# Performance work log

Measured on AMD Instinct MI355X. Metric: run time of the kernel, lower is better.

Reference implementation:

```python
import jax, jax.numpy as jnp
import numpy as np

D_IN, D_HID, D_CLS, N_CLASSES = 1024, 256, 128, 4
CELL_IN = 512
N = 50000


def setup_inputs() -> dict:
    key = jax.random.key(0)
    ks = jax.random.split(key, 20)
    s = 0.02
    inp = {
        "x_path": jax.random.normal(ks[0], (1, N, D_IN), jnp.float32),
        "x_cell": jax.random.normal(ks[1], (1, N, CELL_IN), jnp.float32),
        # wsi_net / cell_net projections
        "wsi_w": jax.random.normal(ks[2], (D_IN, D_HID), jnp.float32) * s,
        "wsi_b": jnp.zeros((D_HID,), jnp.float32),
        "cell_w": jax.random.normal(ks[3], (CELL_IN, D_HID), jnp.float32) * s,
        "cell_b": jnp.zeros((D_HID,), jnp.float32),
        # cross-attention Q/K/V
        "wq_w": jax.random.normal(ks[4], (D_HID, D_HID), jnp.float32) * s,
        "wq_b": jnp.zeros((D_HID,), jnp.float32),
        "wk_w": jax.random.normal(ks[5], (D_HID, D_HID), jnp.float32) * s,
        "wk_b": jnp.zeros((D_HID,), jnp.float32),
        "wv_w": jax.random.normal(ks[6], (D_HID, D_HID), jnp.float32) * s,
        "wv_b": jnp.zeros((D_HID,), jnp.float32),
        # gated attention (L=D=256, n_classes=1)
        "aa_w": jax.random.normal(ks[7], (D_HID, D_HID), jnp.float32) * s,
        "aa_b": jnp.zeros((D_HID,), jnp.float32),
        "ab_w": jax.random.normal(ks[8], (D_HID, D_HID), jnp.float32) * s,
        "ab_b": jnp.zeros((D_HID,), jnp.float32),
        "ac_w": jax.random.normal(ks[9], (D_HID, 1), jnp.float32) * s,
        "ac_b": jnp.zeros((1,), jnp.float32),
        # classifier MLP
        "c1_w": jax.random.normal(ks[10], (D_HID, D_CLS), jnp.float32) * s,
        "c1_b": jnp.zeros((D_CLS,), jnp.float32),
        "c2_w": jax.random.normal(ks[11], (D_CLS, N_CLASSES), jnp.float32) * s,
        "c2_b": jnp.zeros((N_CLASSES,), jnp.float32),
    }
    return inp


def reference(x_path, x_cell, wsi_w, wsi_b, cell_w, cell_b,
              wq_w, wq_b, wk_w, wk_b, wv_w, wv_b,
              aa_w, aa_b, ab_w, ab_b, ac_w, ac_b,
              c1_w, c1_b, c2_w, c2_b):
    xp = x_path[0]            # (N, D_IN)
    xc = x_cell[0]            # (N, CELL_IN)
    # instance-level projections (dropout inactive at eval)
    h_path = jax.nn.relu(xp @ wsi_w + wsi_b)    # (N, d)
    h_cell = jax.nn.relu(xc @ cell_w + cell_b)  # (N, d)
    # cross attention with per-instance seq_len=1 (bmm over N singleton batches)
    q = h_cell @ wq_w + wq_b
    k = h_path @ wk_w + wk_b
    v = h_path @ wv_w + wv_b
    scores = (jnp.einsum('nd,nd->n', q, k) / jnp.sqrt(jnp.float32(q.shape[-1])))[:, None, None]  # (N,1,1)
    attn_w = jax.nn.softmax(scores, axis=-1)     # (N,1,1), trivially ones
    fused = attn_w[:, 0, :] * v                  # (N, d)
    # gated attention MIL pooling
    a = jnp.tanh(fused @ aa_w + aa_b)
    b = jax.nn.sigmoid(fused @ ab_w + ab_b)
    A = (a * b) @ ac_w + ac_b                    # (N, 1)
    A_t = A.T                                    # (1, N)
    pooled = jax.nn.softmax(A_t, axis=1) @ fused # (1, d)
    # classifier MLP
    risk = jax.nn.relu(pooled @ c1_w + c1_b) @ c2_w + c2_b  # (1, n_classes)
    return risk
```

## Files before the change

kernel.cpp:

```cpp
#include <hip/hip_runtime.h>
#include <hip/hip_bf16.h>
#include <math.h>

#define D_IN 1024
#define D_HID 256
#define D_CLS 128
#define N_CLASSES 4
#define N_INST 50000

#define NPAD 50176
#define G1 (NPAD / 64)
#define RG2 128
#define GB (NPAD / RG2)
#define PSTR 258
#define NEG_BIG (-1e30f)

#define ROWS 64
#define NBLK ((N_INST + ROWS - 1) / ROWS)
#define NB2 64
#define CHUNK ((NBLK + NB2 - 1) / NB2)

#define WS_W1T   0u
#define WS_WVT   524288u
#define WS_WAT   655360u
#define WS_WBT   786432u
#define WS_CNT   917504u
#define WS_P1    917760u
#define WS_H     1322304u
#define WS_NEED2 ((size_t)WS_H + 25690112u)
#define WS_P1F   917504u
#define WS_P2F   1724800u

typedef __attribute__((ext_vector_type(8))) short bf16x8;
typedef __attribute__((ext_vector_type(4))) float f32x4;

__device__ __forceinline__ short f2bf(float x) {
    __hip_bfloat16 h = __float2bfloat16(x);
    return *reinterpret_cast<short*>(&h);
}
__device__ __forceinline__ float fast_tanh(float x) {
    float e = __expf(2.f * x);
    return 1.f - 2.f * __builtin_amdgcn_rcpf(e + 1.f);
}
__device__ __forceinline__ float fast_sigmoid(float x) {
    return __builtin_amdgcn_rcpf(1.f + __expf(-x));
}
__device__ __forceinline__ bf16x8 cvt8(float4 a, float4 b) {
    bf16x8 r;
    r[0] = f2bf(a.x); r[1] = f2bf(a.y); r[2] = f2bf(a.z); r[3] = f2bf(a.w);
    r[4] = f2bf(b.x); r[5] = f2bf(b.y); r[6] = f2bf(b.z); r[7] = f2bf(b.w);
    return r;
}
__device__ __forceinline__ bf16x8 cvt8v(f32x4 a, f32x4 b) {
    bf16x8 r;
    r[0] = f2bf(a[0]); r[1] = f2bf(a[1]); r[2] = f2bf(a[2]); r[3] = f2bf(a[3]);
    r[4] = f2bf(b[0]); r[5] = f2bf(b[1]); r[6] = f2bf(b[2]); r[7] = f2bf(b[3]);
    return r;
}
__device__ __forceinline__ bf16x8 load_cvt8(const float* __restrict__ p) {
    return cvt8(*(const float4*)p, *(const float4*)(p + 4));
}
__device__ __forceinline__ void async_ld16(const float* g, float* l) {
    __builtin_amdgcn_global_load_lds(
        (const __attribute__((address_space(1))) void*)g,
        (__attribute__((address_space(3))) void*)l, 16, 0, 0);
}

__global__ void convert_weights(const float* __restrict__ w1, const float* __restrict__ wv,
                                const float* __restrict__ wa, const float* __restrict__ wb,
                                __hip_bfloat16* __restrict__ w1t, __hip_bfloat16* __restrict__ wvt,
                                __hip_bfloat16* __restrict__ wat, __hip_bfloat16* __restrict__ wbt) {
    __shared__ __hip_bfloat16 T[64][68];
    int b = blockIdx.x, tid = threadIdx.x;
    const float* src; __hip_bfloat16* dst; int K, tr, tc;
    if (b < 64) { src = w1; dst = w1t; K = D_IN; tr = b >> 2; tc = b & 3; }
    else {
        int m = (b - 64) >> 4, t = (b - 64) & 15;
        src = (m == 0) ? wv : (m == 1) ? wa : wb;
        dst = (m == 0) ? wvt : (m == 1) ? wat : wbt;
        K = D_HID; tr = t >> 2; tc = t & 3;
    }
    int k0 = tr * 64, n0 = tc * 64;
#pragma unroll
    for (int p = 0; p < 4; p++) {
        int lin = p * 256 + tid;
        int r = lin >> 4;
        int c4 = (lin & 15) << 2;
        float4 v = *(const float4*)(src + (size_t)(k0 + r) * D_HID + n0 + c4);
        T[c4 + 0][r] = __float2bfloat16(v.x);
        T[c4 + 1][r] = __float2bfloat16(v.y);
        T[c4 + 2][r] = __float2bfloat16(v.z);
        T[c4 + 3][r] = __float2bfloat16(v.w);
    }
    __syncthreads();
#pragma unroll
    for (int p = 0; p < 4; p++) {
        int lin = p * 256 + tid;
        int n = lin >> 4;
        int kq = (lin & 15) << 2;
        ushort4 o;
        o.x = *(unsigned short*)&T[n][kq + 0];
        o.y = *(unsigned short*)&T[n][kq + 1];
        o.z = *(unsigned short*)&T[n][kq + 2];
        o.w = *(unsigned short*)&T[n][kq + 3];
        *(ushort4*)(dst + (size_t)(n0 + n) * K + k0 + kq) = o;
    }
}

__global__ __launch_bounds__(256, 3) void mcat_stage1h(const float* __restrict__ xp,
                                                       const __hip_bfloat16* __restrict__ w1t,
                                                       const float* __restrict__ b1,
                                                       __hip_bfloat16* __restrict__ hout) {
    __shared__ float Xs[4][2048];

    const int tid  = threadIdx.x;
    const int wave = tid >> 6;
    const int lane = tid & 63;
    const int quad = lane >> 4;
    const int l16  = lane & 15;
    const int row0 = blockIdx.x * 64;
    const int t128 = blockIdx.x >> 1;
    const int rhalf = blockIdx.x & 1;

    const int dma_rsub = lane >> 3;
    const int dma_gran = (lane & 7) ^ dma_rsub;
    auto stage = [&](int buf, int kc) {
#pragma unroll
        for (int c = 0; c < 2; c++) {
            const int chunk = wave * 2 + c;
            int rg = row0 + chunk * 8 + dma_rsub;
            if (rg > N_INST - 1) rg = N_INST - 1;
            async_ld16(xp + (size_t)rg * D_IN + kc + dma_gran * 4, &Xs[buf][chunk * 256]);
        }
    };

    const __hip_bfloat16* wb[4];
#pragma unroll
    for (int ct = 0; ct < 4; ct++)
        wb[ct] = w1t + (size_t)(wave * 64 + ct * 16 + l16) * D_IN + quad * 8;

    f32x4 acc[4][4];
    f32x4 zero = {0.f, 0.f, 0.f, 0.f};
#pragma unroll
    for (int i = 0; i < 4; i++)
#pragma unroll
        for (int j = 0; j < 4; j++) acc[i][j] = zero;

    stage(0, 0);
    bf16x8 wcur[4];
#pragma unroll
    for (int ct = 0; ct < 4; ct++) wcur[ct] = *(const bf16x8*)(wb[ct]);
    stage(1, 32);
    stage(2, 64);

    const int key = l16 & 7;
#pragma unroll 1
    for (int t = 0; t < 32; t++) {
        if (t == 0)      asm volatile("s_waitcnt vmcnt(4)" ::: "memory");
        else if (t < 29) asm volatile("s_waitcnt vmcnt(2)" ::: "memory");
        else             asm volatile("s_waitcnt vmcnt(0)" ::: "memory");
        __builtin_amdgcn_s_barrier();

        bf16x8 wnx[4];
        if (t < 31) {
#pragma unroll
            for (int ct = 0; ct < 4; ct++)
                wnx[ct] = *(const bf16x8*)(wb[ct] + (t + 1) * 32);
        }
        if (t < 29) stage((t + 3) & 3, (t + 3) * 32);

        const float* bufp = &Xs[t & 3][0];
#pragma unroll
        for (int rt = 0; rt < 4; rt++) {
            const float* rp = bufp + (rt * 16 + l16) * 32;
            f32x4 lo = *(const f32x4*)(rp + (((2 * quad) ^ key) << 2));
            f32x4 hi = *(const f32x4*)(rp + (((2 * quad + 1) ^ key) << 2));
            bf16x8 af = cvt8v(lo, hi);
#pragma unroll
            for (int ct = 0; ct < 4; ct++)
                acc[rt][ct] = __builtin_amdgcn_mfma_f32_16x16x32_bf16(af, wcur[ct], acc[rt][ct], 0, 0, 0);
        }
        if (t < 31) {
#pragma unroll
            for (int ct = 0; ct < 4; ct++) wcur[ct] = wnx[ct];
        }
    }

#pragma unroll
    for (int ct = 0; ct < 4; ct++) {
        const int col = wave * 64 + ct * 16 + l16;
        const float bias = b1[col];
        __hip_bfloat16* hb = hout + (((size_t)(t128 * 8 + (col >> 5)) * 4 + ((col >> 3) & 3)) << 10)
                                  + rhalf * 512 + (col & 7);
#pragma unroll
        for (int rt = 0; rt < 4; rt++)
#pragma unroll
            for (int r = 0; r < 4; r++) {
                int row = rt * 16 + quad * 4 + r;
                hb[row * 8] = __float2bfloat16(fmaxf(acc[rt][ct][r] + bias, 0.f));
            }
    }
}

__global__ __launch_bounds__(512, 1) void mcat_stage2(const __hip_bfloat16* __restrict__ h,
                          const __hip_bfloat16* __restrict__ wvt, const float* __restrict__ bv,
                          const __hip_bfloat16* __restrict__ wat, const float* __restrict__ ba,
                          const __hip_bfloat16* __restrict__ wbt, const float* __restrict__ bb,
                          const float* __restrict__ acw, const float* __restrict__ acb,
                          float* __restrict__ p1, unsigned int* __restrict__ counter,
                          const float* __restrict__ c1w, const float* __restrict__ c1b,
                          const float* __restrict__ c2w, const float* __restrict__ c2b,
                          float* __restrict__ out) {
    __shared__ __hip_bfloat16 Vs[RG2][264];
    __shared__ float Apart[8][RG2];
    __shared__ float ExpW[RG2];
    __shared__ float smx[4];
    __shared__ float scb[GB];
    __shared__ float pooled[D_HID];
    __shared__ float r1v[D_CLS];

    const int tid  = threadIdx.x;
    const int wave = tid >> 6;
    const int lane = tid & 63;
    const int quad = lane >> 4;
    const int l16  = lane & 15;
    const int cb   = wave * 32;
    const int row0 = blockIdx.x * RG2;

    f32x4 acc[8][2];
    f32x4 zero = {0.f, 0.f, 0.f, 0.f};

    const __hip_bfloat16* hb = h + (size_t)blockIdx.x * 32768 + quad * 1024 + l16 * 8;
#pragma unroll
    for (int i = 0; i < 8; i++) { acc[i][0] = zero; acc[i][1] = zero; }
    {
        const __hip_bfloat16* w0 = wvt + (size_t)(cb + l16) * D_HID + quad * 8;
        const __hip_bfloat16* w1p = w0 + 16 * D_HID;
#pragma unroll
        for (int ks = 0; ks < 8; ks++) {
            bf16x8 b0 = *(const bf16x8*)(w0 + ks * 32);
            bf16x8 b1f = *(const bf16x8*)(w1p + ks * 32);
#pragma unroll
            for (int rt = 0; rt < 8; rt++) {
                bf16x8 af = *(const bf16x8*)(hb + ks * 4096 + rt * 128);
                acc[rt][0] = __builtin_amdgcn_mfma_f32_16x16x32_bf16(af, b0, acc[rt][0], 0, 0, 0);
                acc[rt][1] = __builtin_amdgcn_mfma_f32_16x16x32_bf16(af, b1f, acc[rt][1], 0, 0, 0);
            }
        }
    }
#pragma unroll
    for (int ct = 0; ct < 2; ct++) {
        int col = cb + ct * 16 + l16;
        float bias = bv[col];
#pragma unroll
        for (int rt = 0; rt < 8; rt++)
#pragma unroll
            for (int r = 0; r < 4; r++)
                Vs[rt * 16 + quad * 4 + r][col] = __float2bfloat16(acc[rt][ct][r] + bias);
    }
    __syncthreads();

    float a_reg[8][2][4];
#pragma unroll
    for (int i = 0; i < 8; i++) { acc[i][0] = zero; acc[i][1] = zero; }
    {
        const __hip_bfloat16* w0 = wat + (size_t)(cb + l16) * D_HID + quad * 8;
        const __hip_bfloat16* w1p = w0 + 16 * D_HID;
#pragma unroll
        for (int ks = 0; ks < 8; ks++) {
            bf16x8 b0 = *(const bf16x8*)(w0 + ks * 32);
            bf16x8 b1f = *(const bf16x8*)(w1p + ks * 32);
#pragma unroll
            for (int rt = 0; rt < 8; rt++) {
                bf16x8 af = *(const bf16x8*)&Vs[rt * 16 + l16][ks * 32 + quad * 8];
                acc[rt][0] = __builtin_amdgcn_mfma_f32_16x16x32_bf16(af, b0, acc[rt][0], 0, 0, 0);
                acc[rt][1] = __builtin_amdgcn_mfma_f32_16x16x32_bf16(af, b1f, acc[rt][1], 0, 0, 0);
            }
        }
    }
#pragma unroll
    for (int ct = 0; ct < 2; ct++) {
        float bias = ba[cb + ct * 16 + l16];
#pragma unroll
        for (int rt = 0; rt < 8; rt++)
#pragma unroll
            for (int r = 0; r < 4; r++)
                a_reg[rt][ct][r] = fast_tanh(acc[rt][ct][r] + bias);
    }

#pragma unroll
    for (int i = 0; i < 8; i++) { acc[i][0] = zero; acc[i][1] = zero; }
    {
        const __hip_bfloat16* w0 = wbt + (size_t)(cb + l16) * D_HID + quad * 8;
        const __hip_bfloat16* w1p = w0 + 16 * D_HID;
#pragma unroll
        for (int ks = 0; ks < 8; ks++) {
            bf16x8 b0 = *(const bf16x8*)(w0 + ks * 32);
            bf16x8 b1f = *(const bf16x8*)(w1p + ks * 32);
#pragma unroll
            for (int rt = 0; rt < 8; rt++) {
                bf16x8 af = *(const bf16x8*)&Vs[rt * 16 + l16][ks * 32 + quad * 8];
                acc[rt][0] = __builtin_amdgcn_mfma_f32_16x16x32_bf16(af, b0, acc[rt][0], 0, 0, 0);
                acc[rt][1] = __builtin_amdgcn_mfma_f32_16x16x32_bf16(af, b1f, acc[rt][1], 0, 0, 0);
            }
        }
    }
    {
        float acw0 = acw[cb + l16], acw1 = acw[cb + 16 + l16];
        float bb0 = bb[cb + l16],  bb1 = bb[cb + 16 + l16];
        float sp[8][4];
#pragma unroll
        for (int rt = 0; rt < 8; rt++)
#pragma unroll
            for (int r = 0; r < 4; r++) {
                float g0 = a_reg[rt][0][r] * fast_sigmoid(acc[rt][0][r] + bb0);
                float g1 = a_reg[rt][1][r] * fast_sigmoid(acc[rt][1][r] + bb1);
                sp[rt][r] = g0 * acw0 + g1 * acw1;
            }
#pragma unroll
        for (int off = 1; off < 16; off <<= 1)
#pragma unroll
            for (int rt = 0; rt < 8; rt++)
#pragma unroll
                for (int r = 0; r < 4; r++)
                    sp[rt][r] += __shfl_xor(sp[rt][r], off, 16);
        if (l16 == 0) {
#pragma unroll
            for (int rt = 0; rt < 8; rt++)
#pragma unroll
                for (int r = 0; r < 4; r++)
                    Apart[wave][rt * 16 + quad * 4 + r] = sp[rt][r];
        }
    }
    __syncthreads();

    if (tid < 64) {
        float A0 = acb[0], A1 = acb[0];
#pragma unroll
        for (int w = 0; w < 8; w++) { A0 += Apart[w][tid]; A1 += Apart[w][tid + 64]; }
        bool v0 = (row0 + tid) < N_INST;
        bool v1 = (row0 + 64 + tid) < N_INST;
        if (!v0) A0 = NEG_BIG;
        if (!v1) A1 = NEG_BIG;
        float m = fmaxf(A0, A1);
#pragma unroll
        for (int off = 32; off > 0; off >>= 1) m = fmaxf(m, __shfl_xor(m, off));
        float e0 = v0 ? __expf(A0 - m) : 0.f;
        float e1 = v1 ? __expf(A1 - m) : 0.f;
        ExpW[tid] = e0; ExpW[tid + 64] = e1;
        float ssum = e0 + e1;
#pragma unroll
        for (int off = 32; off > 0; off >>= 1) ssum += __shfl_xor(ssum, off);
        if (tid == 0) {
            p1[(size_t)blockIdx.x * PSTR + 0] = m;
            p1[(size_t)blockIdx.x * PSTR + 1] = ssum;
        }
    }
    __syncthreads();
    if (tid < 256) {
        float p = 0.f;
#pragma unroll 8
        for (int n = 0; n < RG2; n++)
            p += ExpW[n] * __bfloat162float(Vs[n][tid]);
        p1[(size_t)blockIdx.x * PSTR + 2 + tid] = p;
    }

    __syncthreads();
    if (tid == 0) {
        __threadfence();
        unsigned int old = __hip_atomic_fetch_add(counter, 1u, __ATOMIC_ACQ_REL, __HIP_MEMORY_SCOPE_AGENT);
        smx[3] = (old == GB - 1) ? 1.f : 0.f;
    }
    __syncthreads();
    if (smx[3] == 0.f) return;
    __threadfence();

    {
        float mloc = NEG_BIG;
        for (int b = tid; b < GB; b += 512) mloc = fmaxf(mloc, p1[(size_t)b * PSTR]);
#pragma unroll
        for (int off = 32; off > 0; off >>= 1) mloc = fmaxf(mloc, __shfl_xor(mloc, off));
        if (lane == 0) ExpW[wave] = mloc;
    }
    __syncthreads();
    if (tid == 0) {
        float M = NEG_BIG;
#pragma unroll
        for (int w = 0; w < 8; w++) M = fmaxf(M, ExpW[w]);
        smx[0] = M;
    }
    __syncthreads();
    {
        float M = smx[0];
        float sl = 0.f;
        for (int b = tid; b < GB; b += 512) {
            float s = __expf(p1[(size_t)b * PSTR] - M);
            scb[b] = s;
            sl += s * p1[(size_t)b * PSTR + 1];
        }
#pragma unroll
        for (int off = 32; off > 0; off >>= 1) sl += __shfl_xor(sl, off);
        if (lane == 0) ExpW[8 + wave] = sl;
    }
    __syncthreads();
    if (tid == 0) {
        float S = 0.f;
#pragma unroll
        for (int w = 0; w < 8; w++) S += ExpW[8 + w];
        smx[1] = S;
    }
    __syncthreads();
    if (tid < 256) {
        float p = 0.f;
        for (int b = 0; b < GB; b++)
            p += scb[b] * p1[(size_t)b * PSTR + 2 + tid];
        pooled[tid] = p / smx[1];
    }
    __syncthreads();
    if (tid < D_CLS) {
        float a2 = c1b[tid];
#pragma unroll 8
        for (int d = 0; d < D_HID; d++)
            a2 += pooled[d] * c1w[(size_t)d * D_CLS + tid];
        r1v[tid] = fmaxf(a2, 0.f);
    }
    __syncthreads();
    if (tid < N_CLASSES) {
        float a2 = c2b[tid];
#pragma unroll 8
        for (int j = 0; j < D_CLS; j++)
            a2 += r1v[j] * c2w[(size_t)j * N_CLASSES + tid];
        out[tid] = a2;
    }
}

__device__ __forceinline__ void gemm256_w8(const __hip_bfloat16 (*S)[264],
                                           const __hip_bfloat16* __restrict__ Wt,
                                           int colbase, int quad, int l16, f32x4 acc[4][2]) {
    f32x4 zero = {0.f, 0.f, 0.f, 0.f};
#pragma unroll
    for (int i = 0; i < 4; i++) { acc[i][0] = zero; acc[i][1] = zero; }
    const __hip_bfloat16* w0 = Wt + (size_t)(colbase + l16) * D_HID + quad * 8;
    const __hip_bfloat16* w1 = w0 + 16 * D_HID;
#pragma unroll
    for (int ks = 0; ks < 8; ks++) {
        bf16x8 af[4];
#pragma unroll
        for (int rt = 0; rt < 4; rt++)
            af[rt] = *(const bf16x8*)&S[rt * 16 + l16][ks * 32 + quad * 8];
        bf16x8 b0 = *(const bf16x8*)(w0 + ks * 32);
        bf16x8 b1 = *(const bf16x8*)(w1 + ks * 32);
#pragma unroll
        for (int rt = 0; rt < 4; rt++) {
            acc[rt][0] = __builtin_amdgcn_mfma_f32_16x16x32_bf16(af[rt], b0, acc[rt][0], 0, 0, 0);
            acc[rt][1] = __builtin_amdgcn_mfma_f32_16x16x32_bf16(af[rt], b1, acc[rt][1], 0, 0, 0);
        }
    }
}

__global__ __launch_bounds__(512, 4) void mcat_mainF(const float* __restrict__ xsrc,
                          const __hip_bfloat16* __restrict__ w1t, const float* __restrict__ b1,
                          const __hip_bfloat16* __restrict__ wvt, const float* __restrict__ bv,
                          const __hip_bfloat16* __restrict__ wat, const float* __restrict__ ba,
                          const __hip_bfloat16* __restrict__ wbt, const float* __restrict__ bb,
                          const float* __restrict__ acw, const float* __restrict__ acb,
                          float* __restrict__ partials) {
    __shared__ __hip_bfloat16 Hs[ROWS][264];
    __shared__ __hip_bfloat16 Vs[ROWS][264];
    __shared__ float Apart[8][ROWS];
    __shared__ float ExpW[ROWS];
    const int tid  = threadIdx.x;
    const int wave = tid >> 6;
    const int lane = tid & 63;
    const int quad = lane >> 4;
    const int l16  = lane & 15;
    const int colbase = wave * 32;
    const int row0 = blockIdx.x * ROWS;
    f32x4 acc[4][2];
    f32x4 zero = {0.f, 0.f, 0.f, 0.f};
#pragma unroll
    for (int i = 0; i < 4; i++) { acc[i][0] = zero; acc[i][1] = zero; }
    const float* xf_base[4];
#pragma unroll
    for (int rt = 0; rt < 4; rt++) {
        int r = row0 + rt * 16 + l16;
        if (r > N_INST - 1) r = N_INST - 1;
        xf_base[rt] = xsrc + (size_t)r * D_IN + quad * 8;
    }
    const __hip_bfloat16* wb0 = w1t + (size_t)(colbase + l16) * D_IN + quad * 8;
    const __hip_bfloat16* wb1 = wb0 + 16 * D_IN;
    for (int kc = 0; kc < D_IN; kc += 32) {
        bf16x8 af[4];
#pragma unroll
        for (int rt = 0; rt < 4; rt++) af[rt] = load_cvt8(xf_base[rt] + kc);
        bf16x8 b0 = *(const bf16x8*)(wb0 + kc);
        bf16x8 b1 = *(const bf16x8*)(wb1 + kc);
#pragma unroll
        for (int rt = 0; rt < 4; rt++) {
            acc[rt][0] = __builtin_amdgcn_mfma_f32_16x16x32_bf16(af[rt], b0, acc[rt][0], 0, 0, 0);
            acc[rt][1] = __builtin_amdgcn_mfma_f32_16x16x32_bf16(af[rt], b1, acc[rt][1], 0, 0, 0);
        }
    }
#pragma unroll
    for (int ct = 0; ct < 2; ct++) {
        int col = colbase + ct * 16 + l16;
        float bias = b1[col];
#pragma unroll
        for (int rt = 0; rt < 4; rt++)
#pragma unroll
            for (int r = 0; r < 4; r++)
                Hs[rt * 16 + quad * 4 + r][col] = __float2bfloat16(fmaxf(acc[rt][ct][r] + bias, 0.f));
    }
    __syncthreads();
    gemm256_w8(Hs, wvt, colbase, quad, l16, acc);
#pragma unroll
    for (int ct = 0; ct < 2; ct++) {
        int col = colbase + ct * 16 + l16;
        float bias = bv[col];
#pragma unroll
        for (int rt = 0; rt < 4; rt++)
#pragma unroll
            for (int r = 0; r < 4; r++)
                Vs[rt * 16 + quad * 4 + r][col] = __float2bfloat16(acc[rt][ct][r] + bias);
    }
    __syncthreads();
    float a_reg[4][2][4];
    gemm256_w8(Vs, wat, colbase, quad, l16, acc);
#pragma unroll
    for (int ct = 0; ct < 2; ct++) {
        float bias = ba[colbase + ct * 16 + l16];
#pragma unroll
        for (int rt = 0; rt < 4; rt++)
#pragma unroll
            for (int r = 0; r < 4; r++)
                a_reg[rt][ct][r] = fast_tanh(acc[rt][ct][r] + bias);
    }
    gemm256_w8(Vs, wbt, colbase, quad, l16, acc);
    {
        float acw0 = acw[colbase + l16];
        float acw1 = acw[colbase + 16 + l16];
        float bias0 = bb[colbase + l16];
        float bias1 = bb[colbase + 16 + l16];
        float sp[4][4];
#pragma unroll
        for (int rt = 0; rt < 4; rt++)
#pragma unroll
            for (int r = 0; r < 4; r++) {
                float g0 = a_reg[rt][0][r] * fast_sigmoid(acc[rt][0][r] + bias0);
                float g1 = a_reg[rt][1][r] * fast_sigmoid(acc[rt][1][r] + bias1);
                sp[rt][r] = g0 * acw0 + g1 * acw1;
            }
#pragma unroll
        for (int off = 1; off < 16; off <<= 1)
#pragma unroll
            for (int rt = 0; rt < 4; rt++)
#pragma unroll
                for (int r = 0; r < 4; r++)
                    sp[rt][r] += __shfl_xor(sp[rt][r], off, 16);
        if (l16 == 0) {
#pragma unroll
            for (int rt = 0; rt < 4; rt++)
#pragma unroll
                for (int r = 0; r < 4; r++)
                    Apart[wave][rt * 16 + quad * 4 + r] = sp[rt][r];
        }
    }
    __syncthreads();
    if (tid < 64) {
        bool valid = (row0 + tid) < N_INST;
        float A = acb[0];
#pragma unroll
        for (int w = 0; w < 8; w++) A += Apart[w][tid];
        if (!valid) A = NEG_BIG;
        float m = A;
#pragma unroll
        for (int off = 32; off > 0; off >>= 1) m = fmaxf(m, __shfl_xor(m, off));
        float e = valid ? __expf(A - m) : 0.f;
        ExpW[tid] = e;
        float ssum = e;
#pragma unroll
        for (int off = 32; off > 0; off >>= 1) ssum += __shfl_xor(ssum, off);
        if (tid == 0) {
            partials[(size_t)blockIdx.x * PSTR + 0] = m;
            partials[(size_t)blockIdx.x * PSTR + 1] = ssum;
        }
    }
    __syncthreads();
    if (tid < 256) {
        float p = 0.f;
#pragma unroll 8
        for (int n = 0; n < 64; n++)
            p += ExpW[n] * __bfloat162float(Vs[n][tid]);
        partials[(size_t)blockIdx.x * PSTR + 2 + tid] = p;
    }
}

__global__ void mcat_fin_a(const float* __restrict__ p1, float* __restrict__ p2) {
    __shared__ float sm[1];
    int g = blockIdx.x, tid = threadIdx.x;
    int lo = g * CHUNK;
    int hi = lo + CHUNK; if (hi > NBLK) hi = NBLK;
    if (tid < 64) {
        float m = NEG_BIG;
        if (lo + tid < hi) m = p1[(size_t)(lo + tid) * PSTR];
#pragma unroll
        for (int off = 32; off > 0; off >>= 1) m = fmaxf(m, __shfl_xor(m, off));
        if (tid == 0) sm[0] = m;
    }
    __syncthreads();
    float M = sm[0];
    float p = 0.f, sacc = 0.f;
    for (int b = lo; b < hi; b++) {
        float sc = __expf(p1[(size_t)b * PSTR] - M);
        sacc += sc * p1[(size_t)b * PSTR + 1];
        p += sc * p1[(size_t)b * PSTR + 2 + tid];
    }
    if (tid == 0) {
        p2[(size_t)g * PSTR + 0] = M;
        p2[(size_t)g * PSTR + 1] = sacc;
    }
    p2[(size_t)g * PSTR + 2 + tid] = p;
}

__global__ void mcat_fin_b(const float* __restrict__ p2,
                           const float* __restrict__ c1w, const float* __restrict__ c1b,
                           const float* __restrict__ c2w, const float* __restrict__ c2b,
                           float* __restrict__ out) {
    __shared__ float sm[2];
    __shared__ float sc[NB2];
    __shared__ float pooled[D_HID];
    __shared__ float r1[D_CLS];
    int tid = threadIdx.x;
    if (tid < 64) {
        float m = p2[(size_t)tid * PSTR];
#pragma unroll
        for (int off = 32; off > 0; off >>= 1) m = fmaxf(m, __shfl_xor(m, off));
        if (tid == 0) sm[0] = m;
    }
    __syncthreads();
    float M = sm[0];
    if (tid < 64) {
        float s = __expf(p2[(size_t)tid * PSTR] - M);
        sc[tid] = s;
        float Ssum = s * p2[(size_t)tid * PSTR + 1];
#pragma unroll
        for (int off = 32; off > 0; off >>= 1) Ssum += __shfl_xor(Ssum, off);
        if (tid == 0) sm[1] = Ssum;
    }
    __syncthreads();
    float S = sm[1];
    float p = 0.f;
#pragma unroll 8
    for (int b = 0; b < NB2; b++)
        p += sc[b] * p2[(size_t)b * PSTR + 2 + tid];
    pooled[tid] = p / S;
    __syncthreads();
    if (tid < D_CLS) {
        float acc = c1b[tid];
#pragma unroll 8
        for (int d = 0; d < D_HID; d++)
            acc += pooled[d] * c1w[(size_t)d * D_CLS + tid];
        r1[tid] = fmaxf(acc, 0.f);
    }
    __syncthreads();
    if (tid < N_CLASSES) {
        float acc = c2b[tid];
#pragma unroll 8
        for (int j = 0; j < D_CLS; j++)
            acc += r1[j] * c2w[(size_t)j * N_CLASSES + tid];
        out[tid] = acc;
    }
}

extern "C" void kernel_launch(void* const* d_in, const int* in_sizes, int n_in,
                              void* d_out, int out_size, void* d_ws, size_t ws_size,
                              hipStream_t stream) {
    const float* xp  = (const float*)d_in[0];
    const float* w1  = (const float*)d_in[2];
    const float* b1  = (const float*)d_in[3];
    const float* wv  = (const float*)d_in[10];
    const float* bv  = (const float*)d_in[11];
    const float* wa  = (const float*)d_in[12];
    const float* ba  = (const float*)d_in[13];
    const float* wb  = (const float*)d_in[14];
    const float* bb  = (const float*)d_in[15];
    const float* acw = (const float*)d_in[16];
    const float* acb = (const float*)d_in[17];
    const float* c1w = (const float*)d_in[18];
    const float* c1b = (const float*)d_in[19];
    const float* c2w = (const float*)d_in[20];
    const float* c2b = (const float*)d_in[21];
    float* out = (float*)d_out;

    char* ws = (char*)d_ws;
    __hip_bfloat16* w1t = (__hip_bfloat16*)(ws + WS_W1T);
    __hip_bfloat16* wvt = (__hip_bfloat16*)(ws + WS_WVT);
    __hip_bfloat16* wat = (__hip_bfloat16*)(ws + WS_WAT);
    __hip_bfloat16* wbt = (__hip_bfloat16*)(ws + WS_WBT);

    hipLaunchKernelGGL(convert_weights, dim3(112), dim3(256), 0, stream,
                       w1, wv, wa, wb, w1t, wvt, wat, wbt);

    if (ws_size >= WS_NEED2) {
        unsigned int* counter = (unsigned int*)(ws + WS_CNT);
        float* p1 = (float*)(ws + WS_P1);
        __hip_bfloat16* h  = (__hip_bfloat16*)(ws + WS_H);
        hipMemsetAsync(counter, 0, 4, stream);
        hipLaunchKernelGGL(mcat_stage1h, dim3(G1), dim3(256), 0, stream, xp, w1t, b1, h);
        hipLaunchKernelGGL(mcat_stage2, dim3(GB), dim3(512), 0, stream,
                           h, wvt, bv, wat, ba, wbt, bb, acw, acb, p1, counter,
                           c1w, c1b, c2w, c2b, out);
    } else {
        float* p1 = (float*)(ws + WS_P1F);
        float* p2 = (float*)(ws + WS_P2F);
        hipLaunchKernelGGL(mcat_mainF, dim3(NBLK), dim3(512), 0, stream,
                           xp, w1t, b1, wvt, bv, wat, ba, wbt, bb, acw, acb, p1);
        hipLaunchKernelGGL(mcat_fin_a, dim3(NB2), dim3(256), 0, stream, p1, p2);
        hipLaunchKernelGGL(mcat_fin_b, dim3(1), dim3(256), 0, stream,
                           p2, c1w, c1b, c2w, c2b, out);
    }
}
```

Baseline: 520.0 us.

## Halve stage-1 row tile and pre-swizzle W1 into MFMA fragment layout

The first-layer GEMM kernel now handles 32 rows per block instead of 64. That doubles the grid, halves the LDS staging buffer and raises launch-bounds occupancy from 3 to 5 blocks. The weight-conversion kernel gains a mode that writes W1 in per-lane MFMA fragment order, so each wave's weight load is one contiguous 16-byte read per lane rather than a strided row gather. The aim is better latency hiding for the memory-bound x_path stream and cheaper weight fetches. The cost is that each W1 fragment is reused across half as many rows, so weight traffic through L2 doubles.

```diff
diff --git a/kernel.cpp b/kernel.cpp
--- a/kernel.cpp
+++ b/kernel.cpp
@@ -9,7 +9,7 @@
 #define N_INST 50000
 
 #define NPAD 50176
-#define G1 (NPAD / 64)
+#define G1I (NPAD / 32)
 #define RG2 128
 #define GB (NPAD / RG2)
 #define PSTR 258
@@ -69,9 +69,27 @@
 __global__ void convert_weights(const float* __restrict__ w1, const float* __restrict__ wv,
                                 const float* __restrict__ wa, const float* __restrict__ wb,
                                 __hip_bfloat16* __restrict__ w1t, __hip_bfloat16* __restrict__ wvt,
-                                __hip_bfloat16* __restrict__ wat, __hip_bfloat16* __restrict__ wbt) {
+                                __hip_bfloat16* __restrict__ wat, __hip_bfloat16* __restrict__ wbt,
+                                int frag) {
     __shared__ __hip_bfloat16 T[64][68];
     int b = blockIdx.x, tid = threadIdx.x;
+    if (frag && b < 64) {
+        const int group = tid >> 6, lane = tid & 63;
+        const int colb = lane & 15;
+        const int kb = (lane >> 4) * 8;
+#pragma unroll
+        for (int p = 0; p < 2; p++) {
+            int tile = b * 8 + group * 2 + p;
+            int kc = tile >> 4, w = (tile >> 2) & 3, ct = tile & 3;
+            int col = w * 64 + ct * 16 + colb;
+            const float* s = w1 + (size_t)(kc * 32 + kb) * D_HID + col;
+            bf16x8 o;
+#pragma unroll
+            for (int j = 0; j < 8; j++) o[j] = f2bf(s[(size_t)j * D_HID]);
+            *(bf16x8*)(w1t + (size_t)tile * 512 + lane * 8) = o;
+        }
+        return;
+    }
     const float* src; __hip_bfloat16* dst; int K, tr, tc;
     if (b < 64) { src = w1; dst = w1t; K = D_IN; tr = b >> 2; tc = b & 3; }
     else {
@@ -107,57 +125,51 @@
     }
 }
 
-__global__ __launch_bounds__(256, 3) void mcat_stage1h(const float* __restrict__ xp,
-                                                       const __hip_bfloat16* __restrict__ w1t,
+__global__ __launch_bounds__(256, 5) void mcat_stage1i(const float* __restrict__ xp,
+                                                       const __hip_bfloat16* __restrict__ w1f,
                                                        const float* __restrict__ b1,
                                                        __hip_bfloat16* __restrict__ hout) {
-    __shared__ float Xs[4][2048];
+    __shared__ float Xs[4][1024];
 
     const int tid  = threadIdx.x;
     const int wave = tid >> 6;
     const int lane = tid & 63;
     const int quad = lane >> 4;
     const int l16  = lane & 15;
-    const int row0 = blockIdx.x * 64;
-    const int t128 = blockIdx.x >> 1;
-    const int rhalf = blockIdx.x & 1;
-
-    const int dma_rsub = lane >> 3;
-    const int dma_gran = (lane & 7) ^ dma_rsub;
-    auto stage = [&](int buf, int kc) {
-#pragma unroll
-        for (int c = 0; c < 2; c++) {
-            const int chunk = wave * 2 + c;
-            int rg = row0 + chunk * 8 + dma_rsub;
-            if (rg > N_INST - 1) rg = N_INST - 1;
-            async_ld16(xp + (size_t)rg * D_IN + kc + dma_gran * 4, &Xs[buf][chunk * 256]);
-        }
-    };
-
-    const __hip_bfloat16* wb[4];
-#pragma unroll
-    for (int ct = 0; ct < 4; ct++)
-        wb[ct] = w1t + (size_t)(wave * 64 + ct * 16 + l16) * D_IN + quad * 8;
-
-    f32x4 acc[4][4];
+    const int row0 = blockIdx.x * 32;
+    const int t128 = blockIdx.x >> 2;
+    const int qtr  = blockIdx.x & 3;
+
+    const int rsub = lane >> 3;
+    const int gran = (lane & 7) ^ rsub;
+    const float* xsrc;
+    {
+        int rg = row0 + wave * 8 + rsub;
+        if (rg > N_INST - 1) rg = N_INST - 1;
+        xsrc = xp + (size_t)rg * D_IN + gran * 4;
+    }
+
+    const __hip_bfloat16* wbase = w1f + (size_t)wave * 4 * 512 + lane * 8;
+
+    f32x4 acc[2][4];
     f32x4 zero = {0.f, 0.f, 0.f, 0.f};
 #pragma unroll
-    for (int i = 0; i < 4; i++)
+    for (int i = 0; i < 2; i++)
 #pragma unroll
         for (int j = 0; j < 4; j++) acc[i][j] = zero;
 
-    stage(0, 0);
+    async_ld16(xsrc + 0, &Xs[0][wave * 256]);
     bf16x8 wcur[4];
 #pragma unroll
-    for (int ct = 0; ct < 4; ct++) wcur[ct] = *(const bf16x8*)(wb[ct]);
-    stage(1, 32);
-    stage(2, 64);
+    for (int ct = 0; ct < 4; ct++) wcur[ct] = *(const bf16x8*)(wbase + (size_t)ct * 512);
+    async_ld16(xsrc + 32, &Xs[1][wave * 256]);
+    async_ld16(xsrc + 64, &Xs[2][wave * 256]);
 
     const int key = l16 & 7;
 #pragma unroll 1
     for (int t = 0; t < 32; t++) {
-        if (t == 0)      asm volatile("s_waitcnt vmcnt(4)" ::: "memory");
-        else if (t < 29) asm volatile("s_waitcnt vmcnt(2)" ::: "memory");
+        if (t == 0)      asm volatile("s_waitcnt vmcnt(2)" ::: "memory");
+        else if (t < 29) asm volatile("s_waitcnt vmcnt(1)" ::: "memory");
         else             asm volatile("s_waitcnt vmcnt(0)" ::: "memory");
         __builtin_amdgcn_s_barrier();
 
@@ -165,13 +177,13 @@
         if (t < 31) {
 #pragma unroll
             for (int ct = 0; ct < 4; ct++)
-                wnx[ct] = *(const bf16x8*)(wb[ct] + (t + 1) * 32);
-        }
-        if (t < 29) stage((t + 3) & 3, (t + 3) * 32);
+                wnx[ct] = *(const bf16x8*)(wbase + (size_t)((t + 1) * 16 + ct) * 512);
+        }
+        if (t < 29) async_ld16(xsrc + (t + 3) * 32, &Xs[(t + 3) & 3][wave * 256]);
 
         const float* bufp = &Xs[t & 3][0];
 #pragma unroll
-        for (int rt = 0; rt < 4; rt++) {
+        for (int rt = 0; rt < 2; rt++) {
             const float* rp = bufp + (rt * 16 + l16) * 32;
             f32x4 lo = *(const f32x4*)(rp + (((2 * quad) ^ key) << 2));
             f32x4 hi = *(const f32x4*)(rp + (((2 * quad + 1) ^ key) << 2));
@@ -191,9 +203,9 @@
         const int col = wave * 64 + ct * 16 + l16;
         const float bias = b1[col];
         __hip_bfloat16* hb = hout + (((size_t)(t128 * 8 + (col >> 5)) * 4 + ((col >> 3) & 3)) << 10)
-                                  + rhalf * 512 + (col & 7);
-#pragma unroll
-        for (int rt = 0; rt < 4; rt++)
+                                  + qtr * 256 + (col & 7);
+#pragma unroll
+        for (int rt = 0; rt < 2; rt++)
 #pragma unroll
             for (int r = 0; r < 4; r++) {
                 int row = rt * 16 + quad * 4 + r;
@@ -698,15 +710,16 @@
     __hip_bfloat16* wat = (__hip_bfloat16*)(ws + WS_WAT);
     __hip_bfloat16* wbt = (__hip_bfloat16*)(ws + WS_WBT);
 
+    const int use_main = (ws_size >= WS_NEED2) ? 1 : 0;
     hipLaunchKernelGGL(convert_weights, dim3(112), dim3(256), 0, stream,
-                       w1, wv, wa, wb, w1t, wvt, wat, wbt);
-
-    if (ws_size >= WS_NEED2) {
+                       w1, wv, wa, wb, w1t, wvt, wat, wbt, use_main);
+
+    if (use_main) {
         unsigned int* counter = (unsigned int*)(ws + WS_CNT);
         float* p1 = (float*)(ws + WS_P1);
         __hip_bfloat16* h  = (__hip_bfloat16*)(ws + WS_H);
         hipMemsetAsync(counter, 0, 4, stream);
-        hipLaunchKernelGGL(mcat_stage1h, dim3(G1), dim3(256), 0, stream, xp, w1t, b1, h);
+        hipLaunchKernelGGL(mcat_stage1i, dim3(G1I), dim3(256), 0, stream, xp, w1t, b1, h);
         hipLaunchKernelGGL(mcat_stage2, dim3(GB), dim3(512), 0, stream,
                            h, wvt, bv, wat, ba, wbt, bb, acw, acb, p1, counter,
                            c1w, c1b, c2w, c2b, out);
```

After: 509.7 us. -2.0%, faster.
